# Performance work log

Hardware: AMD Instinct MI355X
Metric: run time of the kernel (lower is better)

Reference implementation:

```python
import jax, jax.numpy as jnp
from jax import lax
import numpy as np

N, E = 64, 126            # nodes per graph, directed edges (N = E//2 + 1)
BS, T = 32, 512           # batch, train_seq_len
G = BS * T                # total graphs
IN = N * 2                # encoder input_size
H8 = 128 * 8              # hidden_size * 8
OUT = 128                 # output_size (decoder GRU hidden)
L = 2                     # num_layers


def setup_inputs() -> dict:
    key = jax.random.key(0)
    ks = iter(jax.random.split(key, 64))
    def rn(shape, s=0.05):
        return jax.random.normal(next(ks), shape, dtype=jnp.float32) * s
    inp = {}
    inp['x'] = rn((G, N, 2), 1.0)
    inp['edge_index'] = jax.random.randint(next(ks), (2, E), 0, N)
    # GCN params (GCNConv(2,4), GCNConv(4,2), classifier Linear(2,2))
    inp['gcn_w1'] = rn((2, 4), 0.5); inp['gcn_b1'] = rn((4,))
    inp['gcn_w2'] = rn((4, 2), 0.5); inp['gcn_b2'] = rn((2,))
    inp['gcn_cw'] = rn((2, 2), 0.5); inp['gcn_cb'] = rn((2,))
    # Encoder: fl Linear(IN, H8); GRU(H8, H8, L)
    inp['enc_fl_w'] = rn((IN, H8)); inp['enc_fl_b'] = rn((H8,))
    inp['enc_wih'] = rn((L, 3 * H8, H8)); inp['enc_whh'] = rn((L, 3 * H8, H8))
    inp['enc_bih'] = rn((L, 3 * H8)); inp['enc_bhh'] = rn((L, 3 * H8))
    # Decoder: fl Linear(H8, H8); GRU(H8, OUT, L); Linear(OUT, OUT)
    inp['dec_fl_w'] = rn((H8, H8)); inp['dec_fl_b'] = rn((H8,))
    inp['dec_wih0'] = rn((3 * OUT, H8)); inp['dec_wih1'] = rn((3 * OUT, OUT))
    inp['dec_whh'] = rn((L, 3 * OUT, OUT))
    inp['dec_bih'] = rn((L, 3 * OUT)); inp['dec_bhh'] = rn((L, 3 * OUT))
    inp['dec_lin_w'] = rn((OUT, OUT)); inp['dec_lin_b'] = rn((OUT,))
    return inp


def _gcn_conv(h, src, dst, W, b):
    # PyG GCNConv: self-loops + symmetric normalization. h: [G, N, Fin]
    hw = h @ W                                   # [G, N, Fout]
    deg = jnp.ones((N,), hw.dtype).at[dst].add(jnp.ones((E,), hw.dtype))
    dinv = lax.rsqrt(deg)
    norm = dinv[src] * dinv[dst]                 # [E]
    msgs = hw[:, src, :] * norm[None, :, None]   # gather + scale
    agg = jnp.zeros_like(hw).at[:, dst, :].add(msgs)
    agg = agg + hw * (dinv * dinv)[None, :, None]  # self-loop term (norm = 1/deg)
    return agg + b


def _gru_layer(x_seq, wih, whh, bih, bhh):
    # x_seq: [B, T, D]; torch nn.GRU math, h0 = 0
    B = x_seq.shape[0]
    H = whh.shape[1]
    h0 = jnp.zeros((B, H), x_seq.dtype)
    def step(h, x_t):
        gi = x_t @ wih.T + bih
        gh = h @ whh.T + bhh
        i_r, i_z, i_n = jnp.split(gi, 3, axis=-1)
        h_r, h_z, h_n = jnp.split(gh, 3, axis=-1)
        r = jax.nn.sigmoid(i_r + h_r)
        z = jax.nn.sigmoid(i_z + h_z)
        n = jnp.tanh(i_n + r * h_n)
        h_new = (1.0 - z) * n + z * h
        return h_new, h_new
    _, ys = lax.scan(step, h0, jnp.swapaxes(x_seq, 0, 1))
    return jnp.swapaxes(ys, 0, 1)


def reference(x, edge_index, gcn_w1, gcn_b1, gcn_w2, gcn_b2, gcn_cw, gcn_cb,
              enc_fl_w, enc_fl_b, enc_wih, enc_whh, enc_bih, enc_bhh,
              dec_fl_w, dec_fl_b, dec_wih0, dec_wih1, dec_whh, dec_bih, dec_bhh,
              dec_lin_w, dec_lin_b):
    src, dst = edge_index[0], edge_index[1]
    # GCN over all G graphs at once (vectorizes the per-graph Python loop)
    h = jnp.tanh(_gcn_conv(x, src, dst, gcn_w1, gcn_b1))
    h = jnp.tanh(_gcn_conv(h, src, dst, gcn_w2, gcn_b2))
    h = h @ gcn_cw + gcn_cb                      # [G, N, 2]
    res = h.reshape(BS, T, IN)
    # Encoder
    out = jax.nn.relu(res @ enc_fl_w + enc_fl_b)
    for l in range(L):
        out = _gru_layer(out, enc_wih[l], enc_whh[l], enc_bih[l], enc_bhh[l])
    # Decoder (dropout in eval mode = identity)
    d = jax.nn.relu(out @ dec_fl_w + dec_fl_b)
    d = _gru_layer(d, dec_wih0, dec_whh[0], dec_bih[0], dec_bhh[0])
    d = _gru_layer(d, dec_wih1, dec_whh[1], dec_bih[1], dec_bhh[1])
    return d @ dec_lin_w + dec_lin_b             # [BS, T, OUT]
```

## Files before the change

### kernel.cpp

```cpp
#include <hip/hip_runtime.h>

typedef unsigned short u16;
typedef unsigned long long u64;
typedef __attribute__((ext_vector_type(8))) short bf16x8;
typedef __attribute__((ext_vector_type(4))) float f32x4;

#define BSZ 32
#define TT 512
#define GG (BSZ*TT)
#define NNODE 64
#define EE 126
#define H8 1024
#define H3 3072
#define NWAVE 128

__device__ __forceinline__ float b2f(u16 u){
  union { unsigned i; float f; } v; v.i = ((unsigned)u) << 16; return v.f;
}
__device__ __forceinline__ u16 f2b(float f){
  unsigned i = __float_as_uint(f);
  unsigned r = (i + 0x7FFFu + ((i >> 16) & 1u)) >> 16;
  return (u16)r;
}
__device__ __forceinline__ float sigm(float x){ return 1.f/(1.f+__expf(-x)); }
__device__ __forceinline__ float tanh_f(float x){
  float xc = fminf(fmaxf(x, -15.f), 15.f);
  float e = __expf(2.f*xc);
  return (e-1.f)/(e+1.f);
}
__device__ __forceinline__ int prow(int m, int perm){
  return perm ? ((m & (TT-1))*BSZ + (m >> 9)) : m;
}

__global__ __launch_bounds__(256) void detect_dtype(const void* xraw, int* flag){
  __shared__ int cnt;
  if (threadIdx.x == 0) cnt = 0;
  __syncthreads();
  const u16* p = (const u16*)xraw;
  u16 u = p[2*threadIdx.x];
  int e = (u >> 7) & 0xFF;
  int weird = (e < 100 || e > 134) ? 1 : 0;
  atomicAdd(&cnt, weird);
  __syncthreads();
  if (threadIdx.x == 0) *flag = (cnt > 128) ? 1 : 0;
}

__global__ __launch_bounds__(256) void cvt_bf16(const void* __restrict__ in,
                                                u16* __restrict__ out, int n,
                                                const int* __restrict__ flag){
  int i = blockIdx.x*256 + threadIdx.x;
  if (i >= n) return;
  if (*flag) out[i] = f2b(((const float*)in)[i]);
  else       out[i] = ((const u16*)in)[i];
}

__global__ __launch_bounds__(64) void gcn_kernel(
    const u16* __restrict__ x, const int* __restrict__ ei,
    const u16* __restrict__ w1, const u16* __restrict__ b1,
    const u16* __restrict__ w2, const u16* __restrict__ b2,
    const u16* __restrict__ cw, const u16* __restrict__ cb,
    u16* __restrict__ res)
{
  __shared__ int se[EE], de[EE];
  __shared__ float dinv[NNODE];
  __shared__ float nrm[EE];
  __shared__ float hs[NNODE][4];
  const int n = threadIdx.x;
  const int g = blockIdx.x;
  for (int e = n; e < EE; e += 64){ se[e] = ei[e]; de[e] = ei[EE + e]; }
  __syncthreads();
  int cnt = 0;
  for (int e = 0; e < EE; e++) cnt += (de[e] == n) ? 1 : 0;
  float di = rsqrtf(1.0f + (float)cnt);
  dinv[n] = di;
  float x0 = b2f(x[((size_t)g*NNODE + n)*2 + 0]);
  float x1 = b2f(x[((size_t)g*NNODE + n)*2 + 1]);
  float hw[4];
  #pragma unroll
  for (int c = 0; c < 4; c++) hw[c] = x0*b2f(w1[c]) + x1*b2f(w1[4+c]);
  #pragma unroll
  for (int c = 0; c < 4; c++) hs[n][c] = hw[c];
  __syncthreads();
  for (int e = n; e < EE; e += 64) nrm[e] = dinv[se[e]] * dinv[de[e]];
  __syncthreads();
  float selfc = di*di;
  float agg[4];
  #pragma unroll
  for (int c = 0; c < 4; c++) agg[c] = hw[c]*selfc;
  for (int e = 0; e < EE; e++){
    if (de[e] == n){
      float w = nrm[e]; int s = se[e];
      #pragma unroll
      for (int c = 0; c < 4; c++) agg[c] += hs[s][c]*w;
    }
  }
  float h1[4];
  #pragma unroll
  for (int c = 0; c < 4; c++) h1[c] = tanh_f(agg[c] + b2f(b1[c]));
  __syncthreads();
  float hw2[2];
  #pragma unroll
  for (int c = 0; c < 2; c++){
    float s = 0.f;
    #pragma unroll
    for (int k = 0; k < 4; k++) s += h1[k]*b2f(w2[k*2+c]);
    hw2[c] = s;
    hs[n][c] = s;
  }
  __syncthreads();
  float agg2[2] = { hw2[0]*selfc, hw2[1]*selfc };
  for (int e = 0; e < EE; e++){
    if (de[e] == n){
      float w = nrm[e]; int s = se[e];
      agg2[0] += hs[s][0]*w;
      agg2[1] += hs[s][1]*w;
    }
  }
  float h2a = tanh_f(agg2[0] + b2f(b2[0]));
  float h2b = tanh_f(agg2[1] + b2f(b2[1]));
  #pragma unroll
  for (int c = 0; c < 2; c++){
    float o = h2a*b2f(cw[c]) + h2b*b2f(cw[2+c]) + b2f(cb[c]);
    res[(size_t)g*128 + n*2 + c] = f2b(o);
  }
}

__global__ __launch_bounds__(256) void transpose_bf16(
    const u16* __restrict__ in, u16* __restrict__ out, int R, int C)
{
  __shared__ u16 tile[32][33];
  int c0 = blockIdx.x*32, r0 = blockIdx.y*32;
  for (int i = threadIdx.y; i < 32; i += 8)
    tile[i][threadIdx.x] = in[(size_t)(r0+i)*C + c0 + threadIdx.x];
  __syncthreads();
  for (int i = threadIdx.y; i < 32; i += 8)
    out[(size_t)(c0+i)*R + r0 + threadIdx.x] = tile[threadIdx.x][i];
}

__global__ __launch_bounds__(256) void gemm_nt(
    const u16* __restrict__ A, const u16* __restrict__ Bm,
    const u16* __restrict__ bias, void* __restrict__ C,
    int M, int N, int K, int relu, int permA, int permC,
    const int* __restrict__ outflag)
{
  const int wave = threadIdx.x >> 6;
  const int lane = threadIdx.x & 63;
  const int wm = wave >> 1, wn = wave & 1;
  const int q = lane >> 4, lr = lane & 15;
  const int mBase = blockIdx.y*128 + wm*64;
  const int nBase = blockIdx.x*128 + wn*64;
  f32x4 acc[4][4] = {};
  const u16* ap[4]; const u16* bp[4];
  #pragma unroll
  for (int i = 0; i < 4; i++){
    ap[i] = A + (size_t)prow(mBase + i*16 + lr, permA)*K + q*8;
    bp[i] = Bm + (size_t)(nBase + i*16 + lr)*K + q*8;
  }
  for (int kb = 0; kb < K; kb += 32){
    bf16x8 av[4], bv[4];
    #pragma unroll
    for (int i = 0; i < 4; i++){
      av[i] = *(const bf16x8*)ap[i]; bv[i] = *(const bf16x8*)bp[i];
      ap[i] += 32; bp[i] += 32;
    }
    #pragma unroll
    for (int mi = 0; mi < 4; mi++)
      #pragma unroll
      for (int ni = 0; ni < 4; ni++)
        acc[mi][ni] = __builtin_amdgcn_mfma_f32_16x16x32_bf16(av[mi], bv[ni], acc[mi][ni], 0, 0, 0);
  }
  const int of32 = outflag ? *outflag : 0;
  #pragma unroll
  for (int ni = 0; ni < 4; ni++){
    int col = nBase + ni*16 + lr;
    float bb = bias ? b2f(bias[col]) : 0.f;
    #pragma unroll
    for (int mi = 0; mi < 4; mi++){
      #pragma unroll
      for (int r = 0; r < 4; r++){
        int row = prow(mBase + mi*16 + q*4 + r, permC);
        float v = acc[mi][ni][r] + bb;
        if (relu) v = fmaxf(v, 0.f);
        size_t idx = (size_t)row*N + col;
        if (of32) ((float*)C)[idx] = v;
        else      ((u16*)C)[idx]   = f2b(v);
      }
    }
  }
}

__global__ __launch_bounds__(64) void enc_rec(
    const u16* __restrict__ gi,
    const u16* __restrict__ whh,
    const u16* __restrict__ bhh,
    u16* __restrict__ seq,
    int* __restrict__ cnt)
{
  const int wg = blockIdx.x;
  const int lane = threadIdx.x & 63;
  const int q = lane >> 4, lr = lane & 15;
  const int j = (wg >> 1)*16 + lr;
  const int bbase = (wg & 1)*16;
  const int sub = wg & 7;
  const float bh_r = b2f(bhh[j]);
  const float bh_z = b2f(bhh[H8 + j]);
  const float bh_n = b2f(bhh[2*H8 + j]);
  const u16* wp0 = whh + (size_t)(0*H8 + j)*H8 + q*8;
  const u16* wp1 = whh + (size_t)(1*H8 + j)*H8 + q*8;
  const u16* wp2 = whh + (size_t)(2*H8 + j)*H8 + q*8;
  float hreg[4] = {0.f,0.f,0.f,0.f};
  u16 gpre[12];
  #pragma unroll
  for (int r = 0; r < 4; r++){
    size_t row = (size_t)(bbase + q*4 + r)*H3;
    gpre[r]   = gi[row + j];
    gpre[4+r] = gi[row + H8 + j];
    gpre[8+r] = gi[row + 2*H8 + j];
  }
  for (int t = 0; t < TT; t++){
    if (t > 0){
      for (;;){
        int s = 0;
        #pragma unroll
        for (int i = 0; i < 8; i++)
          s += __hip_atomic_load(&cnt[i*TT + (t-1)], __ATOMIC_RELAXED, __HIP_MEMORY_SCOPE_AGENT);
        if (s == NWAVE) break;
        __builtin_amdgcn_s_sleep(1);
      }
      asm volatile("" ::: "memory");
    }
    float gr_[4], gz_[4], gn_[4];
    #pragma unroll
    for (int r = 0; r < 4; r++){
      gr_[r] = b2f(gpre[r]); gz_[r] = b2f(gpre[4+r]); gn_[r] = b2f(gpre[8+r]);
    }
    f32x4 acc0 = {}, acc1 = {}, acc2 = {};
    if (t > 0){
      const u16* ap = seq + (size_t)((t-1)*BSZ + bbase + lr)*H8 + q*8;
      #pragma unroll 8
      for (int kb = 0; kb < 32; kb++){
        const u64* p = (const u64*)(ap + kb*32);
        u64 lo = __hip_atomic_load(p,     __ATOMIC_RELAXED, __HIP_MEMORY_SCOPE_AGENT);
        u64 hi = __hip_atomic_load(p + 1, __ATOMIC_RELAXED, __HIP_MEMORY_SCOPE_AGENT);
        union { u64 v[2]; bf16x8 b; } a; a.v[0] = lo; a.v[1] = hi;
        bf16x8 w0 = *(const bf16x8*)(wp0 + kb*32);
        bf16x8 w1 = *(const bf16x8*)(wp1 + kb*32);
        bf16x8 w2 = *(const bf16x8*)(wp2 + kb*32);
        acc0 = __builtin_amdgcn_mfma_f32_16x16x32_bf16(a.b, w0, acc0, 0,0,0);
        acc1 = __builtin_amdgcn_mfma_f32_16x16x32_bf16(a.b, w1, acc1, 0,0,0);
        acc2 = __builtin_amdgcn_mfma_f32_16x16x32_bf16(a.b, w2, acc2, 0,0,0);
      }
    }
    #pragma unroll
    for (int r = 0; r < 4; r++){
      float rr = sigm(gr_[r] + acc0[r] + bh_r);
      float zz = sigm(gz_[r] + acc1[r] + bh_z);
      float nn = tanh_f(gn_[r] + rr*(acc2[r] + bh_n));
      float hnew = (1.f - zz)*nn + zz*hreg[r];
      hreg[r] = hnew;
      __hip_atomic_store(&seq[(size_t)(t*BSZ + bbase + q*4 + r)*H8 + j], f2b(hnew),
                         __ATOMIC_RELAXED, __HIP_MEMORY_SCOPE_AGENT);
    }
    asm volatile("s_waitcnt vmcnt(0)" ::: "memory");
    if (lane == 0)
      __hip_atomic_fetch_add(&cnt[sub*TT + t], 1, __ATOMIC_RELAXED, __HIP_MEMORY_SCOPE_AGENT);
    if (t + 1 < TT){
      #pragma unroll
      for (int r = 0; r < 4; r++){
        size_t row = (size_t)((t+1)*BSZ + bbase + q*4 + r)*H3;
        gpre[r]   = gi[row + j];
        gpre[4+r] = gi[row + H8 + j];
        gpre[8+r] = gi[row + 2*H8 + j];
      }
    }
  }
}

__global__ __launch_bounds__(256) void dec_rec(
    const u16* __restrict__ gi,
    const u16* __restrict__ whh,
    const u16* __restrict__ bhh,
    u16* __restrict__ seq)
{
  __shared__ u16 hlds[16*136];
  const int bb = blockIdx.x*16;
  const int tid = threadIdx.x;
  const int w = tid >> 6, lane = tid & 63, q = lane >> 4, lr = lane & 15;
  bf16x8 wreg[3][2][4];
  #pragma unroll
  for (int g2 = 0; g2 < 3; g2++)
    #pragma unroll
    for (int nt = 0; nt < 2; nt++){
      int jj = g2*128 + w*32 + nt*16 + lr;
      #pragma unroll
      for (int kb = 0; kb < 4; kb++)
        wreg[g2][nt][kb] = *(const bf16x8*)(whh + (size_t)jj*128 + kb*32 + q*8);
    }
  float bh[3][2];
  #pragma unroll
  for (int g2 = 0; g2 < 3; g2++)
    #pragma unroll
    for (int nt = 0; nt < 2; nt++)
      bh[g2][nt] = b2f(bhh[g2*128 + w*32 + nt*16 + lr]);
  float hreg[2][4] = {};
  u16 gpre[3][2][4];
  #pragma unroll
  for (int r = 0; r < 4; r++){
    size_t row = (size_t)(bb + q*4 + r)*384;
    #pragma unroll
    for (int nt = 0; nt < 2; nt++){
      int jj = w*32 + nt*16 + lr;
      #pragma unroll
      for (int g2 = 0; g2 < 3; g2++)
        gpre[g2][nt][r] = gi[row + g2*128 + jj];
    }
  }
  __syncthreads();
  for (int t = 0; t < TT; t++){
    float gif[3][2][4];
    #pragma unroll
    for (int g2 = 0; g2 < 3; g2++)
      #pragma unroll
      for (int nt = 0; nt < 2; nt++)
        #pragma unroll
        for (int r = 0; r < 4; r++)
          gif[g2][nt][r] = b2f(gpre[g2][nt][r]);
    f32x4 acc[3][2] = {};
    if (t > 0){
      #pragma unroll
      for (int kb = 0; kb < 4; kb++){
        bf16x8 a = *(const bf16x8*)(hlds + lr*136 + kb*32 + q*8);
        #pragma unroll
        for (int g2 = 0; g2 < 3; g2++)
          #pragma unroll
          for (int nt = 0; nt < 2; nt++)
            acc[g2][nt] = __builtin_amdgcn_mfma_f32_16x16x32_bf16(a, wreg[g2][nt][kb], acc[g2][nt], 0,0,0);
      }
    }
    __syncthreads();
    #pragma unroll
    for (int nt = 0; nt < 2; nt++)
      #pragma unroll
      for (int r = 0; r < 4; r++){
        int jj = w*32 + nt*16 + lr;
        int b = bb + q*4 + r;
        float rr = sigm(gif[0][nt][r] + acc[0][nt][r] + bh[0][nt]);
        float zz = sigm(gif[1][nt][r] + acc[1][nt][r] + bh[1][nt]);
        float nn = tanh_f(gif[2][nt][r] + rr*(acc[2][nt][r] + bh[2][nt]));
        float hnew = (1.f - zz)*nn + zz*hreg[nt][r];
        hreg[nt][r] = hnew;
        u16 hb = f2b(hnew);
        hlds[(q*4 + r)*136 + jj] = hb;
        seq[(size_t)(t*BSZ + b)*128 + jj] = hb;
      }
    if (t + 1 < TT){
      #pragma unroll
      for (int r = 0; r < 4; r++){
        size_t row = (size_t)((t+1)*BSZ + bb + q*4 + r)*384;
        #pragma unroll
        for (int nt = 0; nt < 2; nt++){
          int jj = w*32 + nt*16 + lr;
          #pragma unroll
          for (int g2 = 0; g2 < 3; g2++)
            gpre[g2][nt][r] = gi[row + g2*128 + jj];
        }
      }
    }
    __syncthreads();
  }
}

extern "C" void kernel_launch(void* const* d_in, const int* in_sizes, int n_in,
                              void* d_out, int out_size, void* d_ws, size_t ws_size,
                              hipStream_t stream)
{
  const void* x    = d_in[0];
  const int* ei    = (const int*)d_in[1];

  const size_t NEED = (size_t)164 << 20;
  if (ws_size < NEED) return;
  char* wsb = (char*)d_ws;
  const size_t KB = 1024, MB = 1024*1024;

  int* syncv = (int*)wsb;
  int* flag  = (int*)(wsb + 40*KB);
  u16* gw1_c  = (u16*)(wsb + 1*MB + 0);
  u16* gb1_c  = (u16*)(wsb + 1*MB + 64);
  u16* gw2_c  = (u16*)(wsb + 1*MB + 128);
  u16* gb2_c  = (u16*)(wsb + 1*MB + 192);
  u16* gcw_c  = (u16*)(wsb + 1*MB + 256);
  u16* gcb_c  = (u16*)(wsb + 1*MB + 320);
  u16* efb_c  = (u16*)(wsb + 1*MB + 4*KB);
  u16* ebih_c = (u16*)(wsb + 1*MB + 8*KB);
  u16* ebhh_c = (u16*)(wsb + 1*MB + 24*KB);
  u16* dfb_c  = (u16*)(wsb + 1*MB + 40*KB);
  u16* dbih_c = (u16*)(wsb + 1*MB + 45*KB);
  u16* dbhh_c = (u16*)(wsb + 1*MB + 47*KB);
  u16* dlb_c  = (u16*)(wsb + 1*MB + 49*KB);
  u16* wT3    = (u16*)(wsb + 1*MB + 64*KB);
  u16* dlw_c  = (u16*)(wsb + 1*MB + 128*KB);
  u16* efw_c  = (u16*)(wsb + 1*MB + 192*KB);
  u16* wT1    = (u16*)(wsb + 1*MB + 448*KB);
  u16* dfw_c  = (u16*)(wsb + 2*MB);
  u16* wT2    = (u16*)(wsb + 4*MB);
  u16* dwih0_c= (u16*)(wsb + 6*MB);
  u16* dwih1_c= (u16*)(wsb + 7*MB);
  u16* dwhh_c = (u16*)(wsb + 7*MB + 128*KB);
  u16* ewih_c = (u16*)(wsb + 8*MB);
  u16* ewhh_c = (u16*)(wsb + 20*MB);
  u16* res    = (u16*)(wsb + 32*MB);
  u16* bufA   = (u16*)(wsb + 36*MB);
  u16* bufC   = (u16*)(wsb + 68*MB);
  u16* x_c    = bufC;
  u16* giD    = (u16*)(wsb + 100*MB);

  hipMemsetAsync(syncv, 0, 32*KB, stream);
  detect_dtype<<<1, 256, 0, stream>>>(x, flag);

  auto cvt = [&](int idx, u16* dst, int n){
    cvt_bf16<<<(n + 255)/256, 256, 0, stream>>>(d_in[idx], dst, n, flag);
  };
  cvt(0,  x_c,     GG*NNODE*2);
  cvt(2,  gw1_c, 8);  cvt(3, gb1_c, 4);  cvt(4, gw2_c, 8);
  cvt(5,  gb2_c, 2);  cvt(6, gcw_c, 4);  cvt(7, gcb_c, 2);
  cvt(8,  efw_c,   128*1024);   cvt(9,  efb_c, 1024);
  cvt(10, ewih_c,  2*3072*1024);
  cvt(11, ewhh_c,  2*3072*1024);
  cvt(12, ebih_c,  2*3072);     cvt(13, ebhh_c, 2*3072);
  cvt(14, dfw_c,   1024*1024);  cvt(15, dfb_c, 1024);
  cvt(16, dwih0_c, 384*1024);   cvt(17, dwih1_c, 384*128);
  cvt(18, dwhh_c,  2*384*128);
  cvt(19, dbih_c,  2*384);      cvt(20, dbhh_c, 2*384);
  cvt(21, dlw_c,   128*128);    cvt(22, dlb_c, 128);

  transpose_bf16<<<dim3(1024/32, 128/32),  dim3(32,8), 0, stream>>>(efw_c, wT1, 128, 1024);
  transpose_bf16<<<dim3(1024/32, 1024/32), dim3(32,8), 0, stream>>>(dfw_c, wT2, 1024, 1024);
  transpose_bf16<<<dim3(128/32, 128/32),   dim3(32,8), 0, stream>>>(dlw_c, wT3, 128, 128);

  gcn_kernel<<<GG, 64, 0, stream>>>(x_c, ei, gw1_c, gb1_c, gw2_c, gb2_c, gcw_c, gcb_c, res);

  gemm_nt<<<dim3(1024/128, GG/128), 256, 0, stream>>>(res, wT1, efb_c, bufA, GG, 1024, 128, 1, 0, 1, nullptr);
  gemm_nt<<<dim3(3072/128, GG/128), 256, 0, stream>>>(bufA, ewih_c, ebih_c, bufC, GG, 3072, 1024, 0, 1, 1, nullptr);
  enc_rec<<<NWAVE, 64, 0, stream>>>(bufC, ewhh_c, ebhh_c, bufA, syncv);
  gemm_nt<<<dim3(3072/128, GG/128), 256, 0, stream>>>(bufA, ewih_c + 3072*1024, ebih_c + 3072, bufC, GG, 3072, 1024, 0, 1, 1, nullptr);
  enc_rec<<<NWAVE, 64, 0, stream>>>(bufC, ewhh_c + 3072*1024, ebhh_c + 3072, bufA, syncv + 8*TT);

  u16* d0 = bufC;
  gemm_nt<<<dim3(1024/128, GG/128), 256, 0, stream>>>(bufA, wT2, dfb_c, d0, GG, 1024, 1024, 1, 1, 1, nullptr);
  gemm_nt<<<dim3(384/128, GG/128), 256, 0, stream>>>(d0, dwih0_c, dbih_c, giD, GG, 384, 1024, 0, 1, 1, nullptr);
  dec_rec<<<2, 256, 0, stream>>>(giD, dwhh_c, dbhh_c, res);
  gemm_nt<<<dim3(384/128, GG/128), 256, 0, stream>>>(res, dwih1_c, dbih_c + 384, giD, GG, 384, 128, 0, 1, 1, nullptr);
  dec_rec<<<2, 256, 0, stream>>>(giD, dwhh_c + 384*128, dbhh_c + 384, bufA);

  gemm_nt<<<dim3(128/128, GG/128), 256, 0, stream>>>(bufA, wT3, dlb_c, d_out, GG, 128, 128, 0, 1, 0, flag);
}
```

Before: 12.47 ms.

## Pipeline both encoder GRU layers in one persistent kernel, fusing layer-1 input projection

Replaces the two sequential encoder recurrence launches with one persistent kernel of 256 waves. The first 128 waves run layer 0 and the other 128 run layer 1, one timestep behind, synchronised through per-step atomic counters. Layer 1 computes its input projection inline with MFMA from the layer-0 output, which removes the separate large input GEMM and the serialisation between the layers. In exchange, each layer-1 wave does twice the matrix work per step, and the design depends on all 256 waves being co-resident for the spin-wait to make progress. Buffers are reassigned so the layer-1 output does not collide with the decoder intermediates.

```diff
diff --git a/kernel.cpp b/kernel.cpp
--- a/kernel.cpp
+++ b/kernel.cpp
@@ -12,7 +12,6 @@
 #define EE 126
 #define H8 1024
 #define H3 3072
-#define NWAVE 128
 
 __device__ __forceinline__ float b2f(u16 u){
   union { unsigned i; float f; } v; v.i = ((unsigned)u) << 16; return v.f;
@@ -30,6 +29,20 @@
 }
 __device__ __forceinline__ int prow(int m, int perm){
   return perm ? ((m & (TT-1))*BSZ + (m >> 9)) : m;
+}
+__device__ __forceinline__ u64 aload64(const u64* p){
+  return __hip_atomic_load(p, __ATOMIC_RELAXED, __HIP_MEMORY_SCOPE_AGENT);
+}
+__device__ __forceinline__ void spin128(int* base, int t){
+  for (;;){
+    int s = 0;
+    #pragma unroll
+    for (int i = 0; i < 8; i++)
+      s += __hip_atomic_load(&base[i*TT + t], __ATOMIC_RELAXED, __HIP_MEMORY_SCOPE_AGENT);
+    if (s == 128) break;
+    __builtin_amdgcn_s_sleep(1);
+  }
+  asm volatile("" ::: "memory");
 }
 
 __global__ __launch_bounds__(256) void detect_dtype(const void* xraw, int* flag){
@@ -189,89 +202,155 @@
   }
 }
 
-__global__ __launch_bounds__(64) void enc_rec(
+__global__ __launch_bounds__(64) void enc_pipe(
     const u16* __restrict__ gi,
-    const u16* __restrict__ whh,
-    const u16* __restrict__ bhh,
-    u16* __restrict__ seq,
+    const u16* __restrict__ wih1,
+    const u16* __restrict__ whh0,
+    const u16* __restrict__ whh1,
+    const u16* __restrict__ bih1, const u16* __restrict__ bhh0,
+    const u16* __restrict__ bhh1,
+    u16* __restrict__ h0seq,
+    u16* __restrict__ h1seq,
     int* __restrict__ cnt)
 {
-  const int wg = blockIdx.x;
+  const int wid = blockIdx.x;
   const int lane = threadIdx.x & 63;
   const int q = lane >> 4, lr = lane & 15;
-  const int j = (wg >> 1)*16 + lr;
-  const int bbase = (wg & 1)*16;
-  const int sub = wg & 7;
-  const float bh_r = b2f(bhh[j]);
-  const float bh_z = b2f(bhh[H8 + j]);
-  const float bh_n = b2f(bhh[2*H8 + j]);
-  const u16* wp0 = whh + (size_t)(0*H8 + j)*H8 + q*8;
-  const u16* wp1 = whh + (size_t)(1*H8 + j)*H8 + q*8;
-  const u16* wp2 = whh + (size_t)(2*H8 + j)*H8 + q*8;
+  const int sub = wid & 7;
   float hreg[4] = {0.f,0.f,0.f,0.f};
-  u16 gpre[12];
-  #pragma unroll
-  for (int r = 0; r < 4; r++){
-    size_t row = (size_t)(bbase + q*4 + r)*H3;
-    gpre[r]   = gi[row + j];
-    gpre[4+r] = gi[row + H8 + j];
-    gpre[8+r] = gi[row + 2*H8 + j];
-  }
-  for (int t = 0; t < TT; t++){
-    if (t > 0){
-      for (;;){
-        int s = 0;
+  int* c0 = cnt;
+  int* c1 = cnt + 8*TT;
+
+  if (wid < 128){
+    const int jg = wid & 63, half = wid >> 6;
+    const int j = jg*16 + lr, bbase = half*16;
+    const float bh_r = b2f(bhh0[j]);
+    const float bh_z = b2f(bhh0[H8 + j]);
+    const float bh_n = b2f(bhh0[2*H8 + j]);
+    const u16* wp0 = whh0 + (size_t)(0*H8 + j)*H8 + q*8;
+    const u16* wp1 = whh0 + (size_t)(1*H8 + j)*H8 + q*8;
+    const u16* wp2 = whh0 + (size_t)(2*H8 + j)*H8 + q*8;
+    u16 gpre[12];
+    #pragma unroll
+    for (int r = 0; r < 4; r++){
+      size_t row = (size_t)(bbase + q*4 + r)*H3;
+      gpre[r]   = gi[row + j];
+      gpre[4+r] = gi[row + H8 + j];
+      gpre[8+r] = gi[row + 2*H8 + j];
+    }
+    for (int t = 0; t < TT; t++){
+      if (t > 0) spin128(c0, t - 1);
+      float gr_[4], gz_[4], gn_[4];
+      #pragma unroll
+      for (int r = 0; r < 4; r++){
+        gr_[r] = b2f(gpre[r]); gz_[r] = b2f(gpre[4+r]); gn_[r] = b2f(gpre[8+r]);
+      }
+      f32x4 acc0 = {}, acc1 = {}, acc2 = {};
+      if (t > 0){
+        const u16* ap = h0seq + (size_t)((t-1)*BSZ + bbase + lr)*H8 + q*8;
+        #pragma unroll 8
+        for (int kb = 0; kb < 32; kb++){
+          const u64* p = (const u64*)(ap + kb*32);
+          union { u64 v[2]; bf16x8 b; } A; A.v[0] = aload64(p); A.v[1] = aload64(p+1);
+          bf16x8 w0 = *(const bf16x8*)(wp0 + kb*32);
+          bf16x8 w1 = *(const bf16x8*)(wp1 + kb*32);
+          bf16x8 w2 = *(const bf16x8*)(wp2 + kb*32);
+          acc0 = __builtin_amdgcn_mfma_f32_16x16x32_bf16(A.b, w0, acc0, 0,0,0);
+          acc1 = __builtin_amdgcn_mfma_f32_16x16x32_bf16(A.b, w1, acc1, 0,0,0);
+          acc2 = __builtin_amdgcn_mfma_f32_16x16x32_bf16(A.b, w2, acc2, 0,0,0);
+        }
+      }
+      #pragma unroll
+      for (int r = 0; r < 4; r++){
+        float rr = sigm(gr_[r] + acc0[r] + bh_r);
+        float zz = sigm(gz_[r] + acc1[r] + bh_z);
+        float nn = tanh_f(gn_[r] + rr*(acc2[r] + bh_n));
+        float hnew = (1.f - zz)*nn + zz*hreg[r];
+        hreg[r] = hnew;
+        __hip_atomic_store(&h0seq[(size_t)(t*BSZ + bbase + q*4 + r)*H8 + j], f2b(hnew),
+                           __ATOMIC_RELAXED, __HIP_MEMORY_SCOPE_AGENT);
+      }
+      asm volatile("s_waitcnt vmcnt(0)" ::: "memory");
+      if (lane == 0)
+        __hip_atomic_fetch_add(&c0[sub*TT + t], 1, __ATOMIC_RELAXED, __HIP_MEMORY_SCOPE_AGENT);
+      if (t + 1 < TT){
         #pragma unroll
-        for (int i = 0; i < 8; i++)
-          s += __hip_atomic_load(&cnt[i*TT + (t-1)], __ATOMIC_RELAXED, __HIP_MEMORY_SCOPE_AGENT);
-        if (s == NWAVE) break;
-        __builtin_amdgcn_s_sleep(1);
-      }
-      asm volatile("" ::: "memory");
-    }
-    float gr_[4], gz_[4], gn_[4];
-    #pragma unroll
-    for (int r = 0; r < 4; r++){
-      gr_[r] = b2f(gpre[r]); gz_[r] = b2f(gpre[4+r]); gn_[r] = b2f(gpre[8+r]);
-    }
-    f32x4 acc0 = {}, acc1 = {}, acc2 = {};
-    if (t > 0){
-      const u16* ap = seq + (size_t)((t-1)*BSZ + bbase + lr)*H8 + q*8;
-      #pragma unroll 8
-      for (int kb = 0; kb < 32; kb++){
-        const u64* p = (const u64*)(ap + kb*32);
-        u64 lo = __hip_atomic_load(p,     __ATOMIC_RELAXED, __HIP_MEMORY_SCOPE_AGENT);
-        u64 hi = __hip_atomic_load(p + 1, __ATOMIC_RELAXED, __HIP_MEMORY_SCOPE_AGENT);
-        union { u64 v[2]; bf16x8 b; } a; a.v[0] = lo; a.v[1] = hi;
-        bf16x8 w0 = *(const bf16x8*)(wp0 + kb*32);
-        bf16x8 w1 = *(const bf16x8*)(wp1 + kb*32);
-        bf16x8 w2 = *(const bf16x8*)(wp2 + kb*32);
-        acc0 = __builtin_amdgcn_mfma_f32_16x16x32_bf16(a.b, w0, acc0, 0,0,0);
-        acc1 = __builtin_amdgcn_mfma_f32_16x16x32_bf16(a.b, w1, acc1, 0,0,0);
-        acc2 = __builtin_amdgcn_mfma_f32_16x16x32_bf16(a.b, w2, acc2, 0,0,0);
-      }
-    }
-    #pragma unroll
-    for (int r = 0; r < 4; r++){
-      float rr = sigm(gr_[r] + acc0[r] + bh_r);
-      float zz = sigm(gz_[r] + acc1[r] + bh_z);
-      float nn = tanh_f(gn_[r] + rr*(acc2[r] + bh_n));
-      float hnew = (1.f - zz)*nn + zz*hreg[r];
-      hreg[r] = hnew;
-      __hip_atomic_store(&seq[(size_t)(t*BSZ + bbase + q*4 + r)*H8 + j], f2b(hnew),
-                         __ATOMIC_RELAXED, __HIP_MEMORY_SCOPE_AGENT);
-    }
-    asm volatile("s_waitcnt vmcnt(0)" ::: "memory");
-    if (lane == 0)
-      __hip_atomic_fetch_add(&cnt[sub*TT + t], 1, __ATOMIC_RELAXED, __HIP_MEMORY_SCOPE_AGENT);
-    if (t + 1 < TT){
+        for (int r = 0; r < 4; r++){
+          size_t row = (size_t)((t+1)*BSZ + bbase + q*4 + r)*H3;
+          gpre[r]   = gi[row + j];
+          gpre[4+r] = gi[row + H8 + j];
+          gpre[8+r] = gi[row + 2*H8 + j];
+        }
+      }
+    }
+  } else {
+    const int wid2 = wid - 128;
+    const int jg = wid2 & 63, half = wid2 >> 6;
+    const int j = jg*16 + lr, bbase = half*16;
+    const float bir = b2f(bih1[j]);
+    const float biz = b2f(bih1[H8 + j]);
+    const float bin = b2f(bih1[2*H8 + j]);
+    const float bhr = b2f(bhh1[j]);
+    const float bhz = b2f(bhh1[H8 + j]);
+    const float bhn = b2f(bhh1[2*H8 + j]);
+    const u16* ip0 = wih1 + (size_t)(0*H8 + j)*H8 + q*8;
+    const u16* ip1 = wih1 + (size_t)(1*H8 + j)*H8 + q*8;
+    const u16* ip2 = wih1 + (size_t)(2*H8 + j)*H8 + q*8;
+    const u16* hp0 = whh1 + (size_t)(0*H8 + j)*H8 + q*8;
+    const u16* hp1 = whh1 + (size_t)(1*H8 + j)*H8 + q*8;
+    const u16* hp2 = whh1 + (size_t)(2*H8 + j)*H8 + q*8;
+    for (int t = 0; t < TT; t++){
+      spin128(c0, t);
+      if (t > 0) spin128(c1, t - 1);
+      f32x4 aI0 = {}, aI1 = {}, aI2 = {}, aH0 = {}, aH1 = {}, aH2 = {};
+      const u16* a0p = h0seq + (size_t)(t*BSZ + bbase + lr)*H8 + q*8;
+      if (t > 0){
+        const u16* a1p = h1seq + (size_t)((t-1)*BSZ + bbase + lr)*H8 + q*8;
+        #pragma unroll 4
+        for (int kb = 0; kb < 32; kb++){
+          const u64* p0 = (const u64*)(a0p + kb*32);
+          union { u64 v[2]; bf16x8 b; } A0; A0.v[0] = aload64(p0); A0.v[1] = aload64(p0+1);
+          const u64* p1 = (const u64*)(a1p + kb*32);
+          union { u64 v[2]; bf16x8 b; } A1; A1.v[0] = aload64(p1); A1.v[1] = aload64(p1+1);
+          bf16x8 i0 = *(const bf16x8*)(ip0 + kb*32);
+          bf16x8 i1 = *(const bf16x8*)(ip1 + kb*32);
+          bf16x8 i2 = *(const bf16x8*)(ip2 + kb*32);
+          bf16x8 h0v = *(const bf16x8*)(hp0 + kb*32);
+          bf16x8 h1v = *(const bf16x8*)(hp1 + kb*32);
+          bf16x8 h2v = *(const bf16x8*)(hp2 + kb*32);
+          aI0 = __builtin_amdgcn_mfma_f32_16x16x32_bf16(A0.b, i0, aI0, 0,0,0);
+          aI1 = __builtin_amdgcn_mfma_f32_16x16x32_bf16(A0.b, i1, aI1, 0,0,0);
+          aI2 = __builtin_amdgcn_mfma_f32_16x16x32_bf16(A0.b, i2, aI2, 0,0,0);
+          aH0 = __builtin_amdgcn_mfma_f32_16x16x32_bf16(A1.b, h0v, aH0, 0,0,0);
+          aH1 = __builtin_amdgcn_mfma_f32_16x16x32_bf16(A1.b, h1v, aH1, 0,0,0);
+          aH2 = __builtin_amdgcn_mfma_f32_16x16x32_bf16(A1.b, h2v, aH2, 0,0,0);
+        }
+      } else {
+        #pragma unroll 8
+        for (int kb = 0; kb < 32; kb++){
+          const u64* p0 = (const u64*)(a0p + kb*32);
+          union { u64 v[2]; bf16x8 b; } A0; A0.v[0] = aload64(p0); A0.v[1] = aload64(p0+1);
+          bf16x8 i0 = *(const bf16x8*)(ip0 + kb*32);
+          bf16x8 i1 = *(const bf16x8*)(ip1 + kb*32);
+          bf16x8 i2 = *(const bf16x8*)(ip2 + kb*32);
+          aI0 = __builtin_amdgcn_mfma_f32_16x16x32_bf16(A0.b, i0, aI0, 0,0,0);
+          aI1 = __builtin_amdgcn_mfma_f32_16x16x32_bf16(A0.b, i1, aI1, 0,0,0);
+          aI2 = __builtin_amdgcn_mfma_f32_16x16x32_bf16(A0.b, i2, aI2, 0,0,0);
+        }
+      }
       #pragma unroll
       for (int r = 0; r < 4; r++){
-        size_t row = (size_t)((t+1)*BSZ + bbase + q*4 + r)*H3;
-        gpre[r]   = gi[row + j];
-        gpre[4+r] = gi[row + H8 + j];
-        gpre[8+r] = gi[row + 2*H8 + j];
-      }
+        float rr = sigm(aI0[r] + bir + aH0[r] + bhr);
+        float zz = sigm(aI1[r] + biz + aH1[r] + bhz);
+        float nn = tanh_f(aI2[r] + bin + rr*(aH2[r] + bhn));
+        float hnew = (1.f - zz)*nn + zz*hreg[r];
+        hreg[r] = hnew;
+        __hip_atomic_store(&h1seq[(size_t)(t*BSZ + bbase + q*4 + r)*H8 + j], f2b(hnew),
+                           __ATOMIC_RELAXED, __HIP_MEMORY_SCOPE_AGENT);
+      }
+      asm volatile("s_waitcnt vmcnt(0)" ::: "memory");
+      if (lane == 0)
+        __hip_atomic_fetch_add(&c1[sub*TT + t], 1, __ATOMIC_RELAXED, __HIP_MEMORY_SCOPE_AGENT);
     }
   }
 }
@@ -412,7 +491,9 @@
   u16* bufA   = (u16*)(wsb + 36*MB);
   u16* bufC   = (u16*)(wsb + 68*MB);
   u16* x_c    = bufC;
-  u16* giD    = (u16*)(wsb + 100*MB);
+  u16* h1seq  = bufC;
+  u16* d0     = (u16*)(wsb + 102*MB);
+  u16* giD    = (u16*)(wsb + 136*MB);
 
   hipMemsetAsync(syncv, 0, 32*KB, stream);
   detect_dtype<<<1, 256, 0, stream>>>(x, flag);
@@ -441,12 +522,11 @@
 
   gemm_nt<<<dim3(1024/128, GG/128), 256, 0, stream>>>(res, wT1, efb_c, bufA, GG, 1024, 128, 1, 0, 1, nullptr);
   gemm_nt<<<dim3(3072/128, GG/128), 256, 0, stream>>>(bufA, ewih_c, ebih_c, bufC, GG, 3072, 1024, 0, 1, 1, nullptr);
-  enc_rec<<<NWAVE, 64, 0, stream>>>(bufC, ewhh_c, ebhh_c, bufA, syncv);
-  gemm_nt<<<dim3(3072/128, GG/128), 256, 0, stream>>>(bufA, ewih_c + 3072*1024, ebih_c + 3072, bufC, GG, 3072, 1024, 0, 1, 1, nullptr);
-  enc_rec<<<NWAVE, 64, 0, stream>>>(bufC, ewhh_c + 3072*1024, ebhh_c + 3072, bufA, syncv + 8*TT);
-
-  u16* d0 = bufC;
-  gemm_nt<<<dim3(1024/128, GG/128), 256, 0, stream>>>(bufA, wT2, dfb_c, d0, GG, 1024, 1024, 1, 1, 1, nullptr);
+  enc_pipe<<<256, 64, 0, stream>>>(bufC, ewih_c + 3072*1024, ewhh_c, ewhh_c + 3072*1024,
+                                   ebih_c + 3072, ebhh_c, ebhh_c + 3072,
+                                   bufA, h1seq, syncv);
+
+  gemm_nt<<<dim3(1024/128, GG/128), 256, 0, stream>>>(h1seq, wT2, dfb_c, d0, GG, 1024, 1024, 1, 1, 1, nullptr);
   gemm_nt<<<dim3(384/128, GG/128), 256, 0, stream>>>(d0, dwih0_c, dbih_c, giD, GG, 384, 1024, 0, 1, 1, nullptr);
   dec_rec<<<2, 256, 0, stream>>>(giD, dwhh_c, dbhh_c, res);
   gemm_nt<<<dim3(384/128, GG/128), 256, 0, stream>>>(res, dwih1_c, dbih_c + 384, giD, GG, 384, 128, 0, 1, 1, nullptr);
```

Measured after the change: 11.72 ms. 1.06x faster.
